# Performance work log

Measured on AMD Instinct MI355X. Metric: run time of the kernel, lower is better.

## Reference

```python
import jax, jax.numpy as jnp
import numpy as np

N_ENT, N_REL, B, D = 100000, 500, 16, 128
P_NORM = 1
EPS = 1e-12


def _l2_normalize(x):
    # mirrors torch.nn.functional.normalize(x, 2, -1)
    n = jnp.sqrt(jnp.sum(x * x, axis=-1, keepdims=True))
    return x / jnp.maximum(n, EPS)


def setup_inputs() -> dict:
    key = jax.random.key(0)
    k0, k1, k2, k3 = jax.random.split(key, 4)
    # xavier_normal_ init: std = sqrt(2 / (fan_in + fan_out))
    ent_emb = jax.random.normal(k0, (N_ENT, D), dtype=jnp.float32) * np.sqrt(2.0 / (N_ENT + D))
    rel_emb = jax.random.normal(k1, (N_REL, D), dtype=jnp.float32) * np.sqrt(2.0 / (N_REL + D))
    e1 = jax.random.randint(k2, (B,), 0, N_ENT, dtype=jnp.int64)
    rel = jax.random.randint(k3, (B,), 0, N_REL, dtype=jnp.int64)
    X = jnp.zeros((B, D), dtype=jnp.float32)   # unused by forward (as in source)
    A = jnp.zeros((B, B), dtype=jnp.float32)   # unused by forward (as in source)
    return {"e1": e1, "rel": rel, "X": X, "A": A, "ent_emb": ent_emb, "rel_emb": rel_emb}


def reference(e1, rel, X, A, ent_emb, rel_emb) -> jnp.ndarray:
    # e1_embedded = normalize(ent_emb[e1]); rel_embedded = normalize(rel_emb[rel])
    e1_e = _l2_normalize(ent_emb[e1])          # [B, D]
    rel_e = _l2_normalize(rel_emb[rel])        # [B, D]
    node = _l2_normalize(ent_emb)              # [N, D]
    head_add_rel = e1_e + rel_e                # [B, D]
    # broadcast pairwise difference: [B, N, D]
    diff = head_add_rel[:, None, :] - node[None, :, :]
    if P_NORM == 1:
        dist = jnp.sum(jnp.abs(diff), axis=2)              # [B, N]
    else:
        dist = jnp.sum(jnp.abs(diff) ** P_NORM, axis=2) ** (1.0 / P_NORM)
    # loss_name == 'BCELoss' -> softmax over entities
    pred = jax.nn.softmax(dist, axis=-1)       # [B, N]
    return pred
```

## Files before the change

kernel.cpp:

```cpp
#include <hip/hip_runtime.h>
#include <hip/hip_bf16.h>

#define N_ENT 100000
#define NB 16
#define DIM 128
#define TILE 64
#define RSTRIDE 132
#define N_TILES ((N_ENT + TILE - 1) / TILE)

__global__ __launch_bounds__(128) void head_kernel(
    const int* __restrict__ e1, const int* __restrict__ rel,
    const float* __restrict__ ent, const float* __restrict__ relemb,
    float* __restrict__ head)
{
    int b = blockIdx.x, d = threadIdx.x;
    float ev = ent[e1[b] * DIM + d];
    float rv = relemb[rel[b] * DIM + d];
    __shared__ float s1[DIM], s2[DIM];
    s1[d] = ev * ev;
    s2[d] = rv * rv;
    __syncthreads();
    for (int s = 64; s > 0; s >>= 1) {
        if (d < s) { s1[d] += s1[d + s]; s2[d] += s2[d + s]; }
        __syncthreads();
    }
    float ne = fmaxf(sqrtf(s1[0]), 1e-12f);
    float nr = fmaxf(sqrtf(s2[0]), 1e-12f);
    head[b * DIM + d] = ev / ne + rv / nr;
}

__global__ __launch_bounds__(512, 8) void dist_kernel(
    const float* __restrict__ ent, const float* __restrict__ head,
    float* __restrict__ partials, float* __restrict__ out)
{
    __shared__ float ldsRow[TILE * RSTRIDE];
    __shared__ float ldsInv[TILE];

    const int tid  = threadIdx.x;
    const int lane = tid & 63;
    const int wv   = __builtin_amdgcn_readfirstlane(tid >> 6);
    const int bbase = wv * 2;
    const int n0 = blockIdx.x * TILE;
    const float4* __restrict__ hg = (const float4*)head;

    {
        const float4* eg = (const float4*)ent;
        #pragma unroll
        for (int i = 0; i < 4; i++) {
            int g = tid + i * 512;
            int r = g >> 5, c = g & 31;
            int gr = n0 + r;
            if (gr >= N_ENT) gr = N_ENT - 1;
            float4 v = eg[gr * (DIM / 4) + c];
            *(float4*)&ldsRow[r * RSTRIDE + c * 4] = v;
        }
    }
    __syncthreads();

    {
        int r = tid >> 3, q = tid & 7;
        const float* p = &ldsRow[r * RSTRIDE + q * 16];
        float s = 0.f;
        #pragma unroll
        for (int k = 0; k < 4; k++) {
            float4 v = *(const float4*)&p[k * 4];
            s = fmaf(v.x, v.x, s); s = fmaf(v.y, v.y, s);
            s = fmaf(v.z, v.z, s); s = fmaf(v.w, v.w, s);
        }
        s += __shfl_down(s, 4);
        s += __shfl_down(s, 2);
        s += __shfl_down(s, 1);
        if (q == 0) ldsInv[r] = 1.0f / fmaxf(sqrtf(s), 1e-12f);
    }
    __syncthreads();

    const float inv = ldsInv[lane];
    const float* rp = &ldsRow[lane * RSTRIDE];

    float a0 = 0.f, a1 = 0.f;
    #pragma unroll
    for (int j = 0; j < DIM / 4; j++) {
        float4 v  = *(const float4*)&rp[j * 4];
        float4 q0 = hg[(bbase + 0) * (DIM / 4) + j];
        float4 q1 = hg[(bbase + 1) * (DIM / 4) + j];
        a0 += fabsf(fmaf(-v.x, inv, q0.x)) + fabsf(fmaf(-v.y, inv, q0.y))
            + fabsf(fmaf(-v.z, inv, q0.z)) + fabsf(fmaf(-v.w, inv, q0.w));
        a1 += fabsf(fmaf(-v.x, inv, q1.x)) + fabsf(fmaf(-v.y, inv, q1.y))
            + fabsf(fmaf(-v.z, inv, q1.z)) + fabsf(fmaf(-v.w, inv, q1.w));
    }

    const int n = n0 + lane;
    const bool valid = (n < N_ENT);
    float e0 = valid ? __expf(a0) : 0.f;
    float e1 = valid ? __expf(a1) : 0.f;
    if (valid) {
        out[(bbase + 0) * N_ENT + n] = e0;
        out[(bbase + 1) * N_ENT + n] = e1;
    }

#define WRED(x) { x += __shfl_down(x, 32); x += __shfl_down(x, 16); \
                  x += __shfl_down(x, 8);  x += __shfl_down(x, 4);  \
                  x += __shfl_down(x, 2);  x += __shfl_down(x, 1); }
    WRED(e0) WRED(e1)
#undef WRED
    if (lane == 0) {
        partials[(bbase + 0) * N_TILES + blockIdx.x] = e0;
        partials[(bbase + 1) * N_TILES + blockIdx.x] = e1;
    }
}

__global__ __launch_bounds__(256) void scale_kernel(
    float* __restrict__ out, const float* __restrict__ partials)
{
    const int b = blockIdx.y;
    const int tid = threadIdx.x;

    const int i = blockIdx.x * 256 + tid;
    float4 v = make_float4(0.f, 0.f, 0.f, 0.f);
    float4* row = (float4*)&out[b * N_ENT];
    const bool valid = (i < N_ENT / 4);
    if (valid) v = row[i];

    float s = 0.f;
    for (int k = tid; k < N_TILES; k += 256) s += partials[b * N_TILES + k];
    s += __shfl_down(s, 32); s += __shfl_down(s, 16);
    s += __shfl_down(s, 8);  s += __shfl_down(s, 4);
    s += __shfl_down(s, 2);  s += __shfl_down(s, 1);
    __shared__ float red[4];
    if ((tid & 63) == 0) red[tid >> 6] = s;
    __syncthreads();
    const float invS = 1.0f / (red[0] + red[1] + red[2] + red[3]);

    if (valid) {
        v.x *= invS; v.y *= invS; v.z *= invS; v.w *= invS;
        row[i] = v;
    }
}

extern "C" void kernel_launch(void* const* d_in, const int* in_sizes, int n_in,
                              void* d_out, int out_size, void* d_ws, size_t ws_size,
                              hipStream_t stream) {
    const int*   e1     = (const int*)d_in[0];
    const int*   rel    = (const int*)d_in[1];
    const float* ent    = (const float*)d_in[4];
    const float* relemb = (const float*)d_in[5];
    float* out = (float*)d_out;

    float* head     = (float*)d_ws;
    float* partials = (float*)((char*)d_ws + 8192);

    head_kernel<<<16, 128, 0, stream>>>(e1, rel, ent, relemb, head);
    dist_kernel<<<N_TILES, 512, 0, stream>>>(ent, head, partials, out);
    scale_kernel<<<dim3((N_ENT / 4 + 255) / 256, NB), 256, 0, stream>>>(out, partials);
}
```

Before: 109.1 us.

## Split distance work by embedding dimension across waves instead of by batch row

Each wave now loads a 16-float slice of every entity row straight into registers, instead of staging the whole 64-row tile in LDS. The row norm is formed by summing per-wave partial sums of squares through LDS. Each wave then computes partial L1 distances for all 16 batch rows over its slice and writes them to LDS, where they are reduced so each wave finalizes two batch rows. The aim is to remove the full-tile LDS staging and the strided LDS row reads. In exchange it keeps 16 accumulators per thread and needs a 32KB LDS partial buffer, which may reduce occupancy.

```diff
diff --git a/kernel.cpp b/kernel.cpp
--- a/kernel.cpp
+++ b/kernel.cpp
@@ -5,7 +5,7 @@
 #define NB 16
 #define DIM 128
 #define TILE 64
-#define RSTRIDE 132
+#define NWAVE 8
 #define N_TILES ((N_ENT + TILE - 1) / TILE)
 
 __global__ __launch_bounds__(128) void head_kernel(
@@ -33,79 +33,78 @@
     const float* __restrict__ ent, const float* __restrict__ head,
     float* __restrict__ partials, float* __restrict__ out)
 {
-    __shared__ float ldsRow[TILE * RSTRIDE];
-    __shared__ float ldsInv[TILE];
+    __shared__ float ldsSsq[NWAVE][TILE];
+    __shared__ float ldsPart[NWAVE][NB][TILE];
 
     const int tid  = threadIdx.x;
     const int lane = tid & 63;
     const int wv   = __builtin_amdgcn_readfirstlane(tid >> 6);
-    const int bbase = wv * 2;
-    const int n0 = blockIdx.x * TILE;
+    const int n0   = blockIdx.x * TILE;
+    int gr = n0 + lane;
+    if (gr >= N_ENT) gr = N_ENT - 1;
+
+    const float4* __restrict__ eg = (const float4*)ent;
+    float4 seg[4];
+    float ssq = 0.f;
+    #pragma unroll
+    for (int c = 0; c < 4; c++) {
+        seg[c] = eg[gr * 32 + wv * 4 + c];
+        ssq = fmaf(seg[c].x, seg[c].x, ssq);
+        ssq = fmaf(seg[c].y, seg[c].y, ssq);
+        ssq = fmaf(seg[c].z, seg[c].z, ssq);
+        ssq = fmaf(seg[c].w, seg[c].w, ssq);
+    }
+    ldsSsq[wv][lane] = ssq;
+    __syncthreads();
+
+    float t = 0.f;
+    #pragma unroll
+    for (int w = 0; w < NWAVE; w++) t += ldsSsq[w][lane];
+    const float inv = 1.0f / fmaxf(sqrtf(t), 1e-12f);
+
     const float4* __restrict__ hg = (const float4*)head;
-
-    {
-        const float4* eg = (const float4*)ent;
+    float acc[NB];
+    #pragma unroll
+    for (int b = 0; b < NB; b++) acc[b] = 0.f;
+    #pragma unroll
+    for (int c = 0; c < 4; c++) {
+        const float4 v = seg[c];
+        const int jg = wv * 4 + c;
         #pragma unroll
-        for (int i = 0; i < 4; i++) {
-            int g = tid + i * 512;
-            int r = g >> 5, c = g & 31;
-            int gr = n0 + r;
-            if (gr >= N_ENT) gr = N_ENT - 1;
-            float4 v = eg[gr * (DIM / 4) + c];
-            *(float4*)&ldsRow[r * RSTRIDE + c * 4] = v;
+        for (int b = 0; b < NB; b++) {
+            float4 q = hg[b * 32 + jg];
+            acc[b] += fabsf(fmaf(-v.x, inv, q.x)) + fabsf(fmaf(-v.y, inv, q.y))
+                    + fabsf(fmaf(-v.z, inv, q.z)) + fabsf(fmaf(-v.w, inv, q.w));
         }
     }
+
+    #pragma unroll
+    for (int b = 0; b < NB; b++) ldsPart[wv][b][lane] = acc[b];
     __syncthreads();
 
-    {
-        int r = tid >> 3, q = tid & 7;
-        const float* p = &ldsRow[r * RSTRIDE + q * 16];
-        float s = 0.f;
-        #pragma unroll
-        for (int k = 0; k < 4; k++) {
-            float4 v = *(const float4*)&p[k * 4];
-            s = fmaf(v.x, v.x, s); s = fmaf(v.y, v.y, s);
-            s = fmaf(v.z, v.z, s); s = fmaf(v.w, v.w, s);
-        }
-        s += __shfl_down(s, 4);
-        s += __shfl_down(s, 2);
-        s += __shfl_down(s, 1);
-        if (q == 0) ldsInv[r] = 1.0f / fmaxf(sqrtf(s), 1e-12f);
+    const int b0 = 2 * wv, b1 = b0 + 1;
+    float s0 = 0.f, s1 = 0.f;
+    #pragma unroll
+    for (int w = 0; w < NWAVE; w++) {
+        s0 += ldsPart[w][b0][lane];
+        s1 += ldsPart[w][b1][lane];
     }
-    __syncthreads();
-
-    const float inv = ldsInv[lane];
-    const float* rp = &ldsRow[lane * RSTRIDE];
-
-    float a0 = 0.f, a1 = 0.f;
-    #pragma unroll
-    for (int j = 0; j < DIM / 4; j++) {
-        float4 v  = *(const float4*)&rp[j * 4];
-        float4 q0 = hg[(bbase + 0) * (DIM / 4) + j];
-        float4 q1 = hg[(bbase + 1) * (DIM / 4) + j];
-        a0 += fabsf(fmaf(-v.x, inv, q0.x)) + fabsf(fmaf(-v.y, inv, q0.y))
-            + fabsf(fmaf(-v.z, inv, q0.z)) + fabsf(fmaf(-v.w, inv, q0.w));
-        a1 += fabsf(fmaf(-v.x, inv, q1.x)) + fabsf(fmaf(-v.y, inv, q1.y))
-            + fabsf(fmaf(-v.z, inv, q1.z)) + fabsf(fmaf(-v.w, inv, q1.w));
-    }
-
     const int n = n0 + lane;
     const bool valid = (n < N_ENT);
-    float e0 = valid ? __expf(a0) : 0.f;
-    float e1 = valid ? __expf(a1) : 0.f;
+    float e0 = valid ? __expf(s0) : 0.f;
+    float e1 = valid ? __expf(s1) : 0.f;
     if (valid) {
-        out[(bbase + 0) * N_ENT + n] = e0;
-        out[(bbase + 1) * N_ENT + n] = e1;
+        out[b0 * N_ENT + n] = e0;
+        out[b1 * N_ENT + n] = e1;
     }
-
 #define WRED(x) { x += __shfl_down(x, 32); x += __shfl_down(x, 16); \
                   x += __shfl_down(x, 8);  x += __shfl_down(x, 4);  \
                   x += __shfl_down(x, 2);  x += __shfl_down(x, 1); }
     WRED(e0) WRED(e1)
 #undef WRED
     if (lane == 0) {
-        partials[(bbase + 0) * N_TILES + blockIdx.x] = e0;
-        partials[(bbase + 1) * N_TILES + blockIdx.x] = e1;
+        partials[b0 * N_TILES + blockIdx.x] = e0;
+        partials[b1 * N_TILES + blockIdx.x] = e1;
     }
 }
 
```

Result: slower. 123.6 us (+13.3%).
